# Kernel optimization log

Hardware: AMD Instinct MI355X
Metric: run time of the kernel (lower is better)

Reference implementation:

```python
import jax, jax.numpy as jnp
import numpy as np

N_NODES = 50000
W_IN = 256
W_OUT = 256
HEADS = 8
D_HEAD = W_OUT // HEADS
NUM_EDGE = 3
N_EDGES = 800000
NEG_SLOPE = 0.2


def setup_inputs() -> dict:
    key = jax.random.key(0)
    ks = jax.random.split(key, 10)
    x = jax.random.normal(ks[0], (N_NODES, W_IN), dtype=jnp.float32)
    adj = jax.random.randint(ks[1], (NUM_EDGE, 2, N_EDGES), 0, N_NODES, dtype=jnp.int64)
    sw = 1.0 / np.sqrt(W_IN)
    # Per-edge-type GATConv params, stacked on leading edge-type axis
    Ws = jax.random.normal(ks[2], (NUM_EDGE, W_IN, HEADS * D_HEAD), dtype=jnp.float32) * sw
    a_l = jax.random.normal(ks[3], (NUM_EDGE, HEADS, D_HEAD), dtype=jnp.float32) * 0.1
    a_r = jax.random.normal(ks[4], (NUM_EDGE, HEADS, D_HEAD), dtype=jnp.float32) * 0.1
    bias = jnp.zeros((NUM_EDGE, HEADS * D_HEAD), dtype=jnp.float32)
    # Semantic attention layer: Linear(w_out -> 1)
    att_w = jax.random.normal(ks[5], (W_OUT, 1), dtype=jnp.float32) * (1.0 / np.sqrt(W_OUT))
    att_b = jnp.zeros((1,), dtype=jnp.float32)
    return {"x": x, "adj": adj, "Ws": Ws, "a_l": a_l, "a_r": a_r,
            "bias": bias, "att_w": att_w, "att_b": att_b}


def _gat(x, edge_index, W, al, ar, b):
    # x: [N, W_IN]; edge_index: [2, E]; W: [W_IN, H*D]; al/ar: [H, D]; b: [H*D]
    N = x.shape[0]
    h = (x @ W).reshape(N, HEADS, D_HEAD)            # [N, H, D]
    src, dst = edge_index[0], edge_index[1]
    el = jnp.einsum('nhd,hd->nh', h, al)             # src-side scores [N, H]
    er = jnp.einsum('nhd,hd->nh', h, ar)             # dst-side scores [N, H]
    e = jax.nn.leaky_relu(el[src] + er[dst], NEG_SLOPE)   # [E, H]
    # segment softmax over incoming edges of each dst node
    m = jax.ops.segment_max(e, dst, num_segments=N)       # [N, H]
    e = jnp.exp(e - m[dst])
    s = jax.ops.segment_sum(e, dst, num_segments=N)       # [N, H]
    alpha = e / (s[dst] + 1e-9)                           # [E, H]
    out = jax.ops.segment_sum(alpha[:, :, None] * h[src], dst, num_segments=N)
    return out.reshape(N, HEADS * D_HEAD) + b             # concat heads [N, W_OUT]


def reference(x, adj, Ws, a_l, a_r, bias, att_w, att_b):
    outs = [_gat(x, adj[i], Ws[i], a_l[i], a_r[i], bias[i]) for i in range(NUM_EDGE)]
    stacked = jnp.stack(outs, axis=1)                     # [N, T, W_OUT]
    # AttentionLayer: scores = Linear(stacked) viewed as [N, 1, T]; NO softmax (faithful)
    att = (stacked @ att_w + att_b).reshape(-1, 1, NUM_EDGE)  # [N, 1, T]
    return jnp.matmul(att, stacked).squeeze(1)            # [N, W_OUT]
```

## Files before the change

### kernel.cpp

```cpp
#include <hip/hip_runtime.h>

#define N_NODES 50000
#define W_IN    256
#define W_OUT   256
#define HEADS   8
#define NUM_T   3
#define N_EDGES 800000
#define NEG_SLOPE 0.2f

#define NB      128
#define BSH     9
#define BNODES  512
#define P1_EPT  16
#define P1_CHUNK (256 * P1_EPT)
#define P1_BLOCKS ((N_EDGES + P1_CHUNK - 1) / P1_CHUNK)
#define NB_USED ((N_NODES + BNODES - 1) / BNODES)

typedef __attribute__((ext_vector_type(8))) short bf16x8;
typedef __attribute__((ext_vector_type(4))) float f32x4;

__device__ __forceinline__ unsigned short f2b(float f) {
    unsigned u = __float_as_uint(f);
    u = (u + 0x7fffu + ((u >> 16) & 1u)) >> 16;
    return (unsigned short)u;
}

__global__ __launch_bounds__(256) void convert_x(const float* __restrict__ x,
                                                 unsigned short* __restrict__ xb) {
    const size_t i = ((size_t)blockIdx.x * 256 + threadIdx.x) * 4;
    const float4 v = *(const float4*)(x + i);
    ushort4 o;
    o.x = f2b(v.x); o.y = f2b(v.y); o.z = f2b(v.z); o.w = f2b(v.w);
    *(ushort4*)(xb + i) = o;
}

__global__ __launch_bounds__(256) void convert_W(const float* __restrict__ Wsrc,
                                                 unsigned short* __restrict__ Wt) {
    const int t = blockIdx.y;
    const int gid = blockIdx.x * 256 + threadIdx.x;
    const int k = gid >> 8, n = gid & 255;
    Wt[(size_t)t * 65536 + (size_t)n * 256 + k] = f2b(Wsrc[(size_t)t * 65536 + gid]);
}

__global__ __launch_bounds__(256) void p1_hist(const int* __restrict__ adj,
                                               int* __restrict__ bucket_cnt) {
    __shared__ int lh[NB];
    const int t = blockIdx.y;
    const int tid = threadIdx.x;
    if (tid < NB) lh[tid] = 0;
    __syncthreads();

    const int* dstp = adj + (size_t)t * 2 * N_EDGES + N_EDGES;
    const int e0 = blockIdx.x * P1_CHUNK + tid * P1_EPT;
#pragma unroll
    for (int i = 0; i < P1_EPT; ++i) {
        const int e = e0 + i;
        if (e < N_EDGES) atomicAdd(&lh[dstp[e] >> BSH], 1);
    }
    __syncthreads();
    if (tid < NB && lh[tid] > 0) atomicAdd(&bucket_cnt[t * NB + tid], lh[tid]);
}

__global__ __launch_bounds__(128) void p1_scan(const int* __restrict__ bucket_cnt,
                                               int* __restrict__ bucket_ptr,
                                               int* __restrict__ bucket_cur) {
    __shared__ int s[NB];
    const int tid = threadIdx.x;
    for (int t = 0; t < NUM_T; ++t) {
        const int v = bucket_cnt[t * NB + tid];
        s[tid] = v;
        __syncthreads();
        for (int off = 1; off < NB; off <<= 1) {
            int o = (tid >= off) ? s[tid - off] : 0;
            __syncthreads();
            s[tid] += o;
            __syncthreads();
        }
        const int incl = s[tid];
        const int excl = incl - v;
        bucket_ptr[t * (NB + 1) + tid] = excl;
        bucket_cur[t * NB + tid] = excl;
        if (tid == NB - 1) bucket_ptr[t * (NB + 1) + NB] = incl;
        __syncthreads();
    }
}

__global__ __launch_bounds__(256) void p1_scatter(const int* __restrict__ adj,
                                                  int* __restrict__ bucket_cur,
                                                  uint2* __restrict__ part) {
    __shared__ int lh[NB];
    __shared__ int lbase[NB];
    const int t = blockIdx.y;
    const int tid = threadIdx.x;
    if (tid < NB) lh[tid] = 0;
    __syncthreads();

    const int* srcp = adj + (size_t)t * 2 * N_EDGES;
    const int* dstp = srcp + N_EDGES;
    const int e0 = blockIdx.x * P1_CHUNK + tid * P1_EPT;

    int es[P1_EPT], ed[P1_EPT], rk[P1_EPT];
#pragma unroll
    for (int i = 0; i < P1_EPT; ++i) {
        const int e = e0 + i;
        if (e < N_EDGES) {
            es[i] = srcp[e];
            ed[i] = dstp[e];
            rk[i] = atomicAdd(&lh[ed[i] >> BSH], 1);
        } else {
            ed[i] = -1;
        }
    }
    __syncthreads();
    if (tid < NB && lh[tid] > 0)
        lbase[tid] = atomicAdd(&bucket_cur[t * NB + tid], lh[tid]);
    __syncthreads();

    uint2* pt = part + (size_t)t * N_EDGES;
#pragma unroll
    for (int i = 0; i < P1_EPT; ++i) {
        if (ed[i] >= 0) {
            const int b = ed[i] >> BSH;
            pt[lbase[b] + rk[i]] = make_uint2((unsigned)es[i], (unsigned)ed[i]);
        }
    }
}

__global__ __launch_bounds__(256) void p2_csr(const uint2* __restrict__ part,
                                              const int* __restrict__ bucket_ptr,
                                              int* __restrict__ row_ptr_all,
                                              int* __restrict__ csr_all) {
    __shared__ int sc[BNODES];
    const int b = blockIdx.x;
    const int t = blockIdx.y;
    const int tid = threadIdx.x;
    const int lane = tid & 63;
    const int wave = tid >> 6;

    const uint2* pt = part + (size_t)t * N_EDGES;
    int* row_ptr = row_ptr_all + (size_t)t * (N_NODES + 1);
    int* csr = csr_all + (size_t)t * N_EDGES;

    const int bp0 = bucket_ptr[t * (NB + 1) + b];
    const int bp1 = bucket_ptr[t * (NB + 1) + b + 1];
    const int node0 = b * BNODES;
    int nn = N_NODES - node0; if (nn > BNODES) nn = BNODES;

    sc[tid] = 0; sc[tid + 256] = 0;
    __syncthreads();

    for (int idx = bp0 + tid; idx < bp1; idx += 256)
        atomicAdd(&sc[pt[idx].y - node0], 1);
    __syncthreads();

    if (wave == 0) {
        int v[8], ex[8];
        int s = 0;
#pragma unroll
        for (int i = 0; i < 8; ++i) { v[i] = sc[lane * 8 + i]; ex[i] = s; s += v[i]; }
        int run = s;
        for (int off = 1; off < 64; off <<= 1) {
            int o = __shfl_up(run, off);
            if (lane >= off) run += o;
        }
        const int base = run - s;
#pragma unroll
        for (int i = 0; i < 8; ++i) sc[lane * 8 + i] = base + ex[i];
    }
    __syncthreads();

    for (int i = tid; i < nn; i += 256) row_ptr[node0 + i] = bp0 + sc[i];
    if (b == NB_USED - 1 && tid == 0) row_ptr[N_NODES] = N_EDGES;
    __syncthreads();

    for (int idx = bp0 + tid; idx < bp1; idx += 256) {
        const uint2 e = pt[idx];
        const int pos = bp0 + atomicAdd(&sc[e.y - node0], 1);
        csr[pos] = (int)e.x;
    }
}

__global__ __launch_bounds__(256) void gemm_fused(const unsigned short* __restrict__ xb,
                                                  const unsigned short* __restrict__ Wt,
                                                  const float* __restrict__ al,
                                                  const float* __restrict__ ar,
                                                  unsigned short* __restrict__ H,
                                                  float* __restrict__ el,
                                                  float* __restrict__ er) {
    __shared__ unsigned short As[64 * 40];
    __shared__ unsigned short Bs[256 * 40];
    __shared__ float els[64 * 8];
    __shared__ float ers[64 * 8];

    const int tid = threadIdx.x;
    const int wave = tid >> 6;
    const int lane = tid & 63;
    const int quad = lane >> 4;
    const int l16 = lane & 15;
    const int m0 = blockIdx.x * 64;

    f32x4 acc[4][4] = {};

    const int arow = tid >> 2;
    const int achunk = (tid & 3) * 8;
    int gm = m0 + arow;
    if (gm > N_NODES - 1) gm = N_NODES - 1;
    const unsigned short* aptr = xb + (size_t)gm * W_IN + achunk;

    for (int k0 = 0; k0 < W_IN; k0 += 32) {
        const uint4 av = *(const uint4*)(aptr + k0);
        *(uint4*)&As[arow * 40 + achunk] = av;
#pragma unroll
        for (int i = 0; i < 4; ++i) {
            const int idx = i * 256 + tid;
            const int brow = idx >> 2;
            const int bch = (idx & 3) * 8;
            const uint4 bv = *(const uint4*)(Wt + (size_t)brow * W_IN + k0 + bch);
            *(uint4*)&Bs[brow * 40 + bch] = bv;
        }
        __syncthreads();

        bf16x8 af[4], bfr[4];
#pragma unroll
        for (int mi = 0; mi < 4; ++mi)
            af[mi] = *(const bf16x8*)&As[(mi * 16 + l16) * 40 + quad * 8];
#pragma unroll
        for (int ni = 0; ni < 4; ++ni)
            bfr[ni] = *(const bf16x8*)&Bs[(wave * 64 + ni * 16 + l16) * 40 + quad * 8];
#pragma unroll
        for (int mi = 0; mi < 4; ++mi)
#pragma unroll
            for (int ni = 0; ni < 4; ++ni)
                acc[mi][ni] = __builtin_amdgcn_mfma_f32_16x16x32_bf16(
                    af[mi], bfr[ni], acc[mi][ni], 0, 0, 0);
        __syncthreads();
    }

#pragma unroll
    for (int mi = 0; mi < 4; ++mi)
#pragma unroll
        for (int reg = 0; reg < 4; ++reg) {
            const int gr = m0 + mi * 16 + quad * 4 + reg;
            if (gr < N_NODES)
#pragma unroll
                for (int ni = 0; ni < 4; ++ni)
                    H[(size_t)gr * W_OUT + wave * 64 + ni * 16 + l16] =
                        f2b(acc[mi][ni][reg]);
        }

    float al4[4], ar4[4];
#pragma unroll
    for (int ni = 0; ni < 4; ++ni) {
        const int c = wave * 64 + ni * 16 + l16;
        al4[ni] = al[c];
        ar4[ni] = ar[c];
    }
#pragma unroll
    for (int mi = 0; mi < 4; ++mi) {
        float pl[4][2] = {}, pr[4][2] = {};
#pragma unroll
        for (int ni = 0; ni < 4; ++ni) {
            const int hl = ni >> 1;
#pragma unroll
            for (int reg = 0; reg < 4; ++reg) {
                pl[reg][hl] += acc[mi][ni][reg] * al4[ni];
                pr[reg][hl] += acc[mi][ni][reg] * ar4[ni];
            }
        }
#pragma unroll
        for (int off = 1; off < 16; off <<= 1)
#pragma unroll
            for (int reg = 0; reg < 4; ++reg)
#pragma unroll
                for (int hl = 0; hl < 2; ++hl) {
                    pl[reg][hl] += __shfl_xor(pl[reg][hl], off);
                    pr[reg][hl] += __shfl_xor(pr[reg][hl], off);
                }
        if (l16 == 0)
#pragma unroll
            for (int reg = 0; reg < 4; ++reg)
#pragma unroll
                for (int hl = 0; hl < 2; ++hl) {
                    const int row = mi * 16 + quad * 4 + reg;
                    els[row * 8 + wave * 2 + hl] = pl[reg][hl];
                    ers[row * 8 + wave * 2 + hl] = pr[reg][hl];
                }
    }
    __syncthreads();

    int nn = N_NODES - m0; if (nn > 64) nn = 64;
    const int nn8 = nn * 8;
    const int i = tid * 4;
    if (i < nn8) {
        *(float4*)(el + (size_t)m0 * 8 + i) = *(float4*)&els[i];
        *(float4*)(er + (size_t)m0 * 8 + i) = *(float4*)&ers[i];
    }
}

__global__ __launch_bounds__(256) void gat_gather(const int* __restrict__ csr_src,
                                                  const int* __restrict__ row_ptr,
                                                  const float* __restrict__ el,
                                                  const float* __restrict__ er,
                                                  const unsigned short* __restrict__ H,
                                                  float* __restrict__ ot) {
    const int node = (blockIdx.x * blockDim.x + threadIdx.x) >> 6;
    const int lane = threadIdx.x & 63;
    if (node >= N_NODES) return;
    const int hh = lane >> 3;

    const int beg = row_ptr[node];
    const int end = row_ptr[node + 1];
    const float erv = er[(size_t)node * HEADS + hh];

    float4 acc = make_float4(0.f, 0.f, 0.f, 0.f);
    float ssum = 0.f;

    for (int j0 = beg; j0 < end; j0 += 64) {
        int nsrc = end - j0;
        if (nsrc > 64) nsrc = 64;
        int mysrc = 0;
        if (j0 + lane < end) mysrc = csr_src[j0 + lane];

        for (int j = 0; j < nsrc; ++j) {
            const int src = __shfl(mysrc, j);
            float v = el[(size_t)src * HEADS + hh] + erv;
            v = (v > 0.f) ? v : NEG_SLOPE * v;
            const float w = __expf(v);
            const uint2 u = *(const uint2*)(H + (size_t)src * W_OUT + lane * 4);
            acc.x += w * __uint_as_float(u.x << 16);
            acc.y += w * __uint_as_float(u.x & 0xffff0000u);
            acc.z += w * __uint_as_float(u.y << 16);
            acc.w += w * __uint_as_float(u.y & 0xffff0000u);
            ssum += w;
        }
    }

    const float inv = 1.f / (ssum + 1e-9f);
    float4 o = make_float4(acc.x * inv, acc.y * inv, acc.z * inv, acc.w * inv);
    *(float4*)(ot + (size_t)node * W_OUT + lane * 4) = o;
}

__global__ __launch_bounds__(256) void combine(const float* __restrict__ ot0,
                                               const float* __restrict__ ot1,
                                               const float* __restrict__ ot2,
                                               const float* __restrict__ bias,
                                               const float* __restrict__ att_w,
                                               const float* __restrict__ att_b,
                                               float* __restrict__ out) {
    const int gw = (blockIdx.x * blockDim.x + threadIdx.x) >> 6;
    const int lane = threadIdx.x & 63;
    if (gw >= N_NODES) return;

    const float4 aw = *(const float4*)(att_w + lane * 4);
    const size_t base = (size_t)gw * W_OUT + lane * 4;

    float4 v[NUM_T];
    float p[NUM_T];
    const float* ots[NUM_T] = {ot0, ot1, ot2};
#pragma unroll
    for (int t = 0; t < NUM_T; ++t) {
        float4 hv = *(const float4*)(ots[t] + base);
        const float4 bv = *(const float4*)(bias + t * W_OUT + lane * 4);
        hv.x += bv.x; hv.y += bv.y; hv.z += bv.z; hv.w += bv.w;
        v[t] = hv;
        p[t] = hv.x * aw.x + hv.y * aw.y + hv.z * aw.z + hv.w * aw.w;
    }
#pragma unroll
    for (int off = 1; off < 64; off <<= 1) {
        p[0] += __shfl_xor(p[0], off);
        p[1] += __shfl_xor(p[1], off);
        p[2] += __shfl_xor(p[2], off);
    }
    const float ab = att_b[0];
    const float a0 = p[0] + ab, a1 = p[1] + ab, a2 = p[2] + ab;
    float4 o;
    o.x = a0 * v[0].x + a1 * v[1].x + a2 * v[2].x;
    o.y = a0 * v[0].y + a1 * v[1].y + a2 * v[2].y;
    o.z = a0 * v[0].z + a1 * v[1].z + a2 * v[2].z;
    o.w = a0 * v[0].w + a1 * v[1].w + a2 * v[2].w;
    *(float4*)(out + base) = o;
}

extern "C" void kernel_launch(void* const* d_in, const int* in_sizes, int n_in,
                              void* d_out, int out_size, void* d_ws, size_t ws_size,
                              hipStream_t stream) {
    const float* x     = (const float*)d_in[0];
    const int*   adj   = (const int*)d_in[1];
    const float* Ws    = (const float*)d_in[2];
    const float* a_l   = (const float*)d_in[3];
    const float* a_r   = (const float*)d_in[4];
    const float* bias  = (const float*)d_in[5];
    const float* att_w = (const float*)d_in[6];
    const float* att_b = (const float*)d_in[7];
    float* out = (float*)d_out;

    char* w = (char*)d_ws;
    unsigned short* xb = (unsigned short*)w; w += (size_t)N_NODES * W_IN * 2;
    unsigned short* H  = (unsigned short*)w; w += (size_t)N_NODES * W_OUT * 2;
    unsigned short* Wt = (unsigned short*)w; w += (size_t)NUM_T * 65536 * 2;
    float* ot0 = (float*)w; w += (size_t)N_NODES * W_OUT * 4;
    float* ot1 = (float*)w; w += (size_t)N_NODES * W_OUT * 4;
    float* el  = (float*)w; w += (size_t)N_NODES * HEADS * 4;
    float* er  = (float*)w; w += (size_t)N_NODES * HEADS * 4;
    int* csr_src = (int*)w; w += (size_t)NUM_T * N_EDGES * 4;
    int* row_ptr = (int*)w; w += (size_t)NUM_T * (N_NODES + 1) * 4;
    int* bucket_cnt = (int*)w; w += NUM_T * NB * 4;
    int* bucket_ptr = (int*)w; w += NUM_T * (NB + 1) * 4;
    int* bucket_cur = (int*)w; w += NUM_T * NB * 4;
    uint2* part = (uint2*)ot0;

    float* ot[NUM_T] = {ot0, ot1, out};
    const int node_wave_blocks = (N_NODES + 3) / 4;
    const int gemm_blocks = (N_NODES + 63) / 64;

    hipMemsetAsync(bucket_cnt, 0, NUM_T * NB * sizeof(int), stream);
    convert_x<<<12500, 256, 0, stream>>>(x, xb);
    convert_W<<<dim3(256, NUM_T), 256, 0, stream>>>(Ws, Wt);
    p1_hist<<<dim3(P1_BLOCKS, NUM_T), 256, 0, stream>>>(adj, bucket_cnt);
    p1_scan<<<1, 128, 0, stream>>>(bucket_cnt, bucket_ptr, bucket_cur);
    p1_scatter<<<dim3(P1_BLOCKS, NUM_T), 256, 0, stream>>>(adj, bucket_cur, part);
    p2_csr<<<dim3(NB_USED, NUM_T), 256, 0, stream>>>(part, bucket_ptr, row_ptr,
                                                     csr_src);

    for (int t = 0; t < NUM_T; ++t) {
        gemm_fused<<<gemm_blocks, 256, 0, stream>>>(
            xb, Wt + (size_t)t * 65536, a_l + t * 256, a_r + t * 256, H, el, er);
        gat_gather<<<node_wave_blocks, 256, 0, stream>>>(
            csr_src + (size_t)t * N_EDGES, row_ptr + (size_t)t * (N_NODES + 1),
            el, er, H, ot[t]);
    }

    combine<<<node_wave_blocks, 256, 0, stream>>>(ot0, ot1, out, bias, att_w,
                                                  att_b, out);
}
```

Measured before the change: 538.8 us.

## Split gather wave into two edge halves with 16B loads; store per-type outputs as bf16

The gather kernel now has each half-wave process alternate edges, with each lane loading 8 bf16 values (16 bytes) instead of 4. Partial sums are then merged with a cross-half shuffle. This halves the serial per-edge loop length and widens memory requests. The per-type GAT outputs are stored as bf16 instead of fp32, which cuts write and read traffic in gather and combine but adds rounding error to the intermediates. The part buffer aliased to ot0 now lives in a smaller region, and this depends on the workspace layout still fitting.

```diff
diff --git a/kernel.cpp b/kernel.cpp
--- a/kernel.cpp
+++ b/kernel.cpp
@@ -24,6 +24,8 @@
     u = (u + 0x7fffu + ((u >> 16) & 1u)) >> 16;
     return (unsigned short)u;
 }
+__device__ __forceinline__ float blo(unsigned u) { return __uint_as_float(u << 16); }
+__device__ __forceinline__ float bhi(unsigned u) { return __uint_as_float(u & 0xffff0000u); }
 
 __global__ __launch_bounds__(256) void convert_x(const float* __restrict__ x,
                                                  unsigned short* __restrict__ xb) {
@@ -302,47 +304,63 @@
                                                   const float* __restrict__ el,
                                                   const float* __restrict__ er,
                                                   const unsigned short* __restrict__ H,
-                                                  float* __restrict__ ot) {
+                                                  unsigned short* __restrict__ ot) {
     const int node = (blockIdx.x * blockDim.x + threadIdx.x) >> 6;
     const int lane = threadIdx.x & 63;
     if (node >= N_NODES) return;
-    const int hh = lane >> 3;
+    const int half = lane >> 5;
+    const int d8 = lane & 31;
+    const int hh = d8 >> 2;
 
     const int beg = row_ptr[node];
     const int end = row_ptr[node + 1];
     const float erv = er[(size_t)node * HEADS + hh];
 
-    float4 acc = make_float4(0.f, 0.f, 0.f, 0.f);
+    float acc[8] = {};
     float ssum = 0.f;
 
     for (int j0 = beg; j0 < end; j0 += 64) {
-        int nsrc = end - j0;
-        if (nsrc > 64) nsrc = 64;
+        int navail = end - j0;
+        if (navail > 64) navail = 64;
         int mysrc = 0;
         if (j0 + lane < end) mysrc = csr_src[j0 + lane];
 
-        for (int j = 0; j < nsrc; ++j) {
-            const int src = __shfl(mysrc, j);
+        const int npairs = (navail + 1) >> 1;
+        for (int p = 0; p < npairs; ++p) {
+            const int ei = 2 * p + half;
+            const int src = __shfl(mysrc, ei);
             float v = el[(size_t)src * HEADS + hh] + erv;
             v = (v > 0.f) ? v : NEG_SLOPE * v;
-            const float w = __expf(v);
-            const uint2 u = *(const uint2*)(H + (size_t)src * W_OUT + lane * 4);
-            acc.x += w * __uint_as_float(u.x << 16);
-            acc.y += w * __uint_as_float(u.x & 0xffff0000u);
-            acc.z += w * __uint_as_float(u.y << 16);
-            acc.w += w * __uint_as_float(u.y & 0xffff0000u);
+            const float w = (ei < navail) ? __expf(v) : 0.f;
+            const uint4 u = *(const uint4*)(H + (size_t)src * W_OUT + d8 * 8);
+            acc[0] += w * blo(u.x);
+            acc[1] += w * bhi(u.x);
+            acc[2] += w * blo(u.y);
+            acc[3] += w * bhi(u.y);
+            acc[4] += w * blo(u.z);
+            acc[5] += w * bhi(u.z);
+            acc[6] += w * blo(u.w);
+            acc[7] += w * bhi(u.w);
             ssum += w;
         }
     }
 
-    const float inv = 1.f / (ssum + 1e-9f);
-    float4 o = make_float4(acc.x * inv, acc.y * inv, acc.z * inv, acc.w * inv);
-    *(float4*)(ot + (size_t)node * W_OUT + lane * 4) = o;
-}
-
-__global__ __launch_bounds__(256) void combine(const float* __restrict__ ot0,
-                                               const float* __restrict__ ot1,
-                                               const float* __restrict__ ot2,
+#pragma unroll
+    for (int i = 0; i < 8; ++i) acc[i] += __shfl_xor(acc[i], 32);
+    ssum += __shfl_xor(ssum, 32);
+
+    if (half == 0) {
+        const float inv = 1.f / (ssum + 1e-9f);
+        unsigned short o8[8];
+#pragma unroll
+        for (int i = 0; i < 8; ++i) o8[i] = f2b(acc[i] * inv);
+        *(uint4*)(ot + (size_t)node * W_OUT + d8 * 8) = *(const uint4*)o8;
+    }
+}
+
+__global__ __launch_bounds__(256) void combine(const unsigned short* __restrict__ ot0,
+                                               const unsigned short* __restrict__ ot1,
+                                               const unsigned short* __restrict__ ot2,
                                                const float* __restrict__ bias,
                                                const float* __restrict__ att_w,
                                                const float* __restrict__ att_b,
@@ -356,12 +374,16 @@
 
     float4 v[NUM_T];
     float p[NUM_T];
-    const float* ots[NUM_T] = {ot0, ot1, ot2};
+    const unsigned short* ots[NUM_T] = {ot0, ot1, ot2};
 #pragma unroll
     for (int t = 0; t < NUM_T; ++t) {
-        float4 hv = *(const float4*)(ots[t] + base);
+        const uint2 u = *(const uint2*)(ots[t] + base);
         const float4 bv = *(const float4*)(bias + t * W_OUT + lane * 4);
-        hv.x += bv.x; hv.y += bv.y; hv.z += bv.z; hv.w += bv.w;
+        float4 hv;
+        hv.x = blo(u.x) + bv.x;
+        hv.y = bhi(u.x) + bv.y;
+        hv.z = blo(u.y) + bv.z;
+        hv.w = bhi(u.y) + bv.w;
         v[t] = hv;
         p[t] = hv.x * aw.x + hv.y * aw.y + hv.z * aw.z + hv.w * aw.w;
     }
@@ -398,8 +420,9 @@
     unsigned short* xb = (unsigned short*)w; w += (size_t)N_NODES * W_IN * 2;
     unsigned short* H  = (unsigned short*)w; w += (size_t)N_NODES * W_OUT * 2;
     unsigned short* Wt = (unsigned short*)w; w += (size_t)NUM_T * 65536 * 2;
-    float* ot0 = (float*)w; w += (size_t)N_NODES * W_OUT * 4;
-    float* ot1 = (float*)w; w += (size_t)N_NODES * W_OUT * 4;
+    unsigned short* ot0 = (unsigned short*)w; w += (size_t)N_NODES * W_OUT * 2;
+    unsigned short* ot1 = (unsigned short*)w; w += (size_t)N_NODES * W_OUT * 2;
+    unsigned short* ot2 = (unsigned short*)w; w += (size_t)N_NODES * W_OUT * 2;
     float* el  = (float*)w; w += (size_t)N_NODES * HEADS * 4;
     float* er  = (float*)w; w += (size_t)N_NODES * HEADS * 4;
     int* csr_src = (int*)w; w += (size_t)NUM_T * N_EDGES * 4;
@@ -409,7 +432,7 @@
     int* bucket_cur = (int*)w; w += NUM_T * NB * 4;
     uint2* part = (uint2*)ot0;
 
-    float* ot[NUM_T] = {ot0, ot1, out};
+    unsigned short* ot[NUM_T] = {ot0, ot1, ot2};
     const int node_wave_blocks = (N_NODES + 3) / 4;
     const int gemm_blocks = (N_NODES + 63) / 64;
 
@@ -430,6 +453,6 @@
             el, er, H, ot[t]);
     }
 
-    combine<<<node_wave_blocks, 256, 0, stream>>>(ot0, ot1, out, bias, att_w,
+    combine<<<node_wave_blocks, 256, 0, stream>>>(ot0, ot1, ot2, bias, att_w,
                                                   att_b, out);
 }
```

Measured after the change: 523.3 us. 1.03x faster.
